# Kernel tuning notes

Hardware: AMD Instinct MI355X
Metric: run time of the kernel (lower is better)

The kernel has to match this reference:

```python
import jax, jax.numpy as jnp
import numpy as np

N_NODES = 4096

def _gcn_conv(x, edge_index, W, b):
    # PyG GCNConv: x' = D^-1/2 (A + I) D^-1/2 (x @ W) + b
    n = x.shape[0]
    self_loops = jnp.arange(n, dtype=edge_index.dtype)
    src = jnp.concatenate([edge_index[0], self_loops])  # message sources
    dst = jnp.concatenate([edge_index[1], self_loops])  # aggregation targets
    xw = x @ W  # [N, 8]
    deg = jax.ops.segment_sum(jnp.ones_like(dst, dtype=xw.dtype), dst, num_segments=n)
    dinv = jnp.where(deg > 0, jax.lax.rsqrt(deg), 0.0)
    norm = dinv[src] * dinv[dst]  # [E+N]
    msg = xw[src] * norm[:, None]  # gather + scale
    out = jax.ops.segment_sum(msg, dst, num_segments=n)  # scatter-add
    return out + b


def setup_inputs() -> dict:
    key = jax.random.key(0)
    k1, k2, k3, k4 = jax.random.split(key, 4)
    n, e, y_dim, hid = N_NODES, 131072, 4096, 8
    x = jax.random.normal(k1, (n, 1), dtype=jnp.float32)
    edge_index = jax.random.randint(k2, (2, e), 0, n, dtype=jnp.int64)
    W1 = jax.random.normal(k3, (1, hid), dtype=jnp.float32)  # fan_in=1
    b1 = jnp.zeros((hid,), dtype=jnp.float32)
    Wr = jax.random.normal(k4, (n * hid, y_dim), dtype=jnp.float32) / np.sqrt(n * hid)
    br = jnp.zeros((y_dim,), dtype=jnp.float32)
    return {"x": x, "edge_index": edge_index, "W1": W1, "b1": b1, "Wr": Wr, "br": br}


def reference(x, edge_index, W1, b1, Wr, br):
    h = _gcn_conv(x, edge_index, W1, b1)        # [N, 8]
    h = jax.nn.relu(h.reshape(-1))               # [N*8]
    return h @ Wr + br                           # [y_dim]
```

## Files before the change

### kernel.cpp

```cpp
#include <hip/hip_runtime.h>

#define N_NODES 4096
#define HID 8
#define N_EDGES 131072
#define YDIM 4096
#define K_TOT (N_NODES * HID)
#define KC 128
#define GEMV_BLOCK 256

__global__ __launch_bounds__(256) void k_init(float* __restrict__ deg,
                                              float* __restrict__ t,
                                              float* __restrict__ out,
                                              const float* __restrict__ br) {
  int i = blockIdx.x * blockDim.x + threadIdx.x;
  if (i < N_NODES) { deg[i] = 1.0f; t[i] = 0.0f; }
  if (i < YDIM) out[i] = br[i];
}

__global__ __launch_bounds__(256) void k_deg(const int* __restrict__ ei,
                                             float* __restrict__ deg) {
  int e = blockIdx.x * blockDim.x + threadIdx.x;
  if (e < N_EDGES) {
    int d = ei[N_EDGES + e];
    atomicAdd(&deg[d], 1.0f);
  }
}

__global__ __launch_bounds__(256) void k_dinv(const float* __restrict__ deg,
                                              float* __restrict__ dinv) {
  int i = blockIdx.x * blockDim.x + threadIdx.x;
  if (i < N_NODES) dinv[i] = rsqrtf(deg[i]);
}

__global__ __launch_bounds__(256) void k_scatter(const int* __restrict__ ei,
                                                 const float* __restrict__ x,
                                                 const float* __restrict__ dinv,
                                                 float* __restrict__ t) {
  int e = blockIdx.x * blockDim.x + threadIdx.x;
  if (e < N_EDGES) {
    int s = ei[e];
    int d = ei[N_EDGES + e];
    atomicAdd(&t[d], x[s] * dinv[s]);
  }
}

__global__ __launch_bounds__(256) void k_h(const float* __restrict__ x,
                                           const float* __restrict__ dinv,
                                           const float* __restrict__ t,
                                           const float* __restrict__ W1,
                                           const float* __restrict__ b1,
                                           float* __restrict__ h) {
  int i = blockIdx.x * blockDim.x + threadIdx.x;
  if (i < N_NODES) {
    float di = dinv[i];
    float s = di * (t[i] + x[i] * di);
#pragma unroll
    for (int j = 0; j < HID; ++j) {
      float v = s * W1[j] + b1[j];
      h[i * HID + j] = v > 0.0f ? v : 0.0f;
    }
  }
}

__global__ __launch_bounds__(GEMV_BLOCK) void k_gemv(const float* __restrict__ Wr,
                                                     const float* __restrict__ h,
                                                     float* __restrict__ out) {
  __shared__ float hs[KC];
  __shared__ int ks[KC];
  __shared__ int cnt;
  const int tid = threadIdx.x;
  const int cg = blockIdx.x & 3;
  const int ck = blockIdx.x >> 2;
  const int k0 = ck * KC;

  if (tid == 0) cnt = 0;
  __syncthreads();
  if (tid < KC) {
    float v = h[k0 + tid];
    if (v != 0.0f) {
      int p = atomicAdd(&cnt, 1);
      hs[p] = v;
      ks[p] = tid;
    }
  }
  __syncthreads();

  const int n = cnt;
  const int col = cg * (GEMV_BLOCK * 4) + tid * 4;
  const float* base = Wr + (size_t)k0 * YDIM + col;
  float ax = 0.f, ay = 0.f, az = 0.f, aw = 0.f;
  for (int q = 0; q < n; ++q) {
    float hv = hs[q];
    int kk = ks[q];
    const float4 w = *(const float4*)(base + (size_t)kk * YDIM);
    ax += hv * w.x;
    ay += hv * w.y;
    az += hv * w.z;
    aw += hv * w.w;
  }
  atomicAdd(&out[col + 0], ax);
  atomicAdd(&out[col + 1], ay);
  atomicAdd(&out[col + 2], az);
  atomicAdd(&out[col + 3], aw);
}

extern "C" void kernel_launch(void* const* d_in, const int* in_sizes, int n_in,
                              void* d_out, int out_size, void* d_ws, size_t ws_size,
                              hipStream_t stream) {
  const float* x  = (const float*)d_in[0];
  const int*   ei = (const int*)d_in[1];
  const float* W1 = (const float*)d_in[2];
  const float* b1 = (const float*)d_in[3];
  const float* Wr = (const float*)d_in[4];
  const float* br = (const float*)d_in[5];
  float* out = (float*)d_out;

  float* deg  = (float*)d_ws;
  float* dinv = deg + N_NODES;
  float* t    = dinv + N_NODES;
  float* h    = t + N_NODES;

  k_init   <<<(N_NODES + 255) / 256, 256, 0, stream>>>(deg, t, out, br);
  k_deg    <<<(N_EDGES + 255) / 256, 256, 0, stream>>>(ei, deg);
  k_dinv   <<<(N_NODES + 255) / 256, 256, 0, stream>>>(deg, dinv);
  k_scatter<<<(N_EDGES + 255) / 256, 256, 0, stream>>>(ei, x, dinv, t);
  k_h      <<<(N_NODES + 255) / 256, 256, 0, stream>>>(x, dinv, t, W1, b1, h);
  k_gemv   <<<4 * (K_TOT / KC), GEMV_BLOCK, 0, stream>>>(Wr, h, out);
}
```

Baseline: 677.4 us.

## Globally compact nonzero ReLU outputs and unroll sparse GEMV for more loads in flight

The hidden-activation kernel now builds one global list of positive ReLU entries, storing their row offsets and values through an atomic counter. The GEMV splits that list evenly across 256 chunks, replacing the old per-block shared-memory compaction of fixed 128-row slices. This balances work between blocks. The inner loop is unrolled by four with separate accumulators so more float4 loads of Wr are outstanding at once. The cost is an extra global atomic per node, row order that varies from run to run, and a fixed shared buffer of 160 entries that assumes no chunk gets more than that.

Measured after the change: 687.1 us. No clear change (+1.4%).

```diff
diff --git a/kernel.cpp b/kernel.cpp
--- a/kernel.cpp
+++ b/kernel.cpp
@@ -5,25 +5,23 @@
 #define N_EDGES 131072
 #define YDIM 4096
 #define K_TOT (N_NODES * HID)
-#define KC 128
+#define NCHUNK 256
 #define GEMV_BLOCK 256
 
 __global__ __launch_bounds__(256) void k_init(float* __restrict__ deg,
                                               float* __restrict__ t,
                                               float* __restrict__ out,
-                                              const float* __restrict__ br) {
+                                              const float* __restrict__ br,
+                                              int* __restrict__ nnz) {
   int i = blockIdx.x * blockDim.x + threadIdx.x;
-  if (i < N_NODES) { deg[i] = 1.0f; t[i] = 0.0f; }
-  if (i < YDIM) out[i] = br[i];
+  if (i < N_NODES) { deg[i] = 1.0f; t[i] = 0.0f; out[i] = br[i]; }
+  if (i == 0) *nnz = 0;
 }
 
 __global__ __launch_bounds__(256) void k_deg(const int* __restrict__ ei,
                                              float* __restrict__ deg) {
   int e = blockIdx.x * blockDim.x + threadIdx.x;
-  if (e < N_EDGES) {
-    int d = ei[N_EDGES + e];
-    atomicAdd(&deg[d], 1.0f);
-  }
+  if (e < N_EDGES) atomicAdd(&deg[ei[N_EDGES + e]], 1.0f);
 }
 
 __global__ __launch_bounds__(256) void k_dinv(const float* __restrict__ deg,
@@ -44,64 +42,82 @@
   }
 }
 
-__global__ __launch_bounds__(256) void k_h(const float* __restrict__ x,
-                                           const float* __restrict__ dinv,
-                                           const float* __restrict__ t,
-                                           const float* __restrict__ W1,
-                                           const float* __restrict__ b1,
-                                           float* __restrict__ h) {
+__global__ __launch_bounds__(256) void k_hc(const float* __restrict__ x,
+                                            const float* __restrict__ dinv,
+                                            const float* __restrict__ t,
+                                            const float* __restrict__ W1,
+                                            const float* __restrict__ b1,
+                                            int* __restrict__ nnz,
+                                            int* __restrict__ nzk,
+                                            float* __restrict__ nzv) {
   int i = blockIdx.x * blockDim.x + threadIdx.x;
-  if (i < N_NODES) {
-    float di = dinv[i];
-    float s = di * (t[i] + x[i] * di);
+  if (i >= N_NODES) return;
+  float di = dinv[i];
+  float s = di * (t[i] + x[i] * di);
+  float v[HID];
+  int nloc = 0;
 #pragma unroll
-    for (int j = 0; j < HID; ++j) {
-      float v = s * W1[j] + b1[j];
-      h[i * HID + j] = v > 0.0f ? v : 0.0f;
+  for (int j = 0; j < HID; ++j) {
+    float u = s * W1[j] + b1[j];
+    v[j] = u;
+    nloc += (u > 0.0f) ? 1 : 0;
+  }
+  int p = atomicAdd(nnz, nloc);
+#pragma unroll
+  for (int j = 0; j < HID; ++j) {
+    if (v[j] > 0.0f) {
+      nzk[p] = (i * HID + j) * YDIM;
+      nzv[p] = v[j];
+      ++p;
     }
   }
 }
 
 __global__ __launch_bounds__(GEMV_BLOCK) void k_gemv(const float* __restrict__ Wr,
-                                                     const float* __restrict__ h,
+                                                     const int* __restrict__ nnzp,
+                                                     const int* __restrict__ nzk,
+                                                     const float* __restrict__ nzv,
                                                      float* __restrict__ out) {
-  __shared__ float hs[KC];
-  __shared__ int ks[KC];
-  __shared__ int cnt;
+  __shared__ float hs[160];
+  __shared__ int ks[160];
   const int tid = threadIdx.x;
   const int cg = blockIdx.x & 3;
   const int ck = blockIdx.x >> 2;
-  const int k0 = ck * KC;
-
-  if (tid == 0) cnt = 0;
-  __syncthreads();
-  if (tid < KC) {
-    float v = h[k0 + tid];
-    if (v != 0.0f) {
-      int p = atomicAdd(&cnt, 1);
-      hs[p] = v;
-      ks[p] = tid;
-    }
-  }
+  const int nnz = *nnzp;
+  const int qs = (ck * nnz) >> 8;
+  const int qe = ((ck + 1) * nnz) >> 8;
+  const int cnt = qe - qs;
+  if (tid < cnt) { hs[tid] = nzv[qs + tid]; ks[tid] = nzk[qs + tid]; }
   __syncthreads();
 
-  const int n = cnt;
   const int col = cg * (GEMV_BLOCK * 4) + tid * 4;
-  const float* base = Wr + (size_t)k0 * YDIM + col;
-  float ax = 0.f, ay = 0.f, az = 0.f, aw = 0.f;
-  for (int q = 0; q < n; ++q) {
-    float hv = hs[q];
-    int kk = ks[q];
-    const float4 w = *(const float4*)(base + (size_t)kk * YDIM);
-    ax += hv * w.x;
-    ay += hv * w.y;
-    az += hv * w.z;
-    aw += hv * w.w;
+  const float* base = Wr + col;
+  float4 a0 = {0, 0, 0, 0}, a1 = {0, 0, 0, 0}, a2 = {0, 0, 0, 0}, a3 = {0, 0, 0, 0};
+  int q = 0;
+  for (; q + 4 <= cnt; q += 4) {
+    float h0 = hs[q], h1 = hs[q + 1], h2 = hs[q + 2], h3 = hs[q + 3];
+    const float4 w0 = *(const float4*)(base + (size_t)(unsigned)ks[q]);
+    const float4 w1 = *(const float4*)(base + (size_t)(unsigned)ks[q + 1]);
+    const float4 w2 = *(const float4*)(base + (size_t)(unsigned)ks[q + 2]);
+    const float4 w3 = *(const float4*)(base + (size_t)(unsigned)ks[q + 3]);
+    a0.x += h0 * w0.x; a0.y += h0 * w0.y; a0.z += h0 * w0.z; a0.w += h0 * w0.w;
+    a1.x += h1 * w1.x; a1.y += h1 * w1.y; a1.z += h1 * w1.z; a1.w += h1 * w1.w;
+    a2.x += h2 * w2.x; a2.y += h2 * w2.y; a2.z += h2 * w2.z; a2.w += h2 * w2.w;
+    a3.x += h3 * w3.x; a3.y += h3 * w3.y; a3.z += h3 * w3.z; a3.w += h3 * w3.w;
   }
-  atomicAdd(&out[col + 0], ax);
-  atomicAdd(&out[col + 1], ay);
-  atomicAdd(&out[col + 2], az);
-  atomicAdd(&out[col + 3], aw);
+  for (; q < cnt; ++q) {
+    float h0 = hs[q];
+    const float4 w0 = *(const float4*)(base + (size_t)(unsigned)ks[q]);
+    a0.x += h0 * w0.x; a0.y += h0 * w0.y; a0.z += h0 * w0.z; a0.w += h0 * w0.w;
+  }
+  float rx = a0.x + a1.x + a2.x + a3.x;
+  float ry = a0.y + a1.y + a2.y + a3.y;
+  float rz = a0.z + a1.z + a2.z + a3.z;
+  float rw = a0.w + a1.w + a2.w + a3.w;
+  atomicAdd(&out[col + 0], rx);
+  atomicAdd(&out[col + 1], ry);
+  atomicAdd(&out[col + 2], rz);
+  atomicAdd(&out[col + 3], rw);
 }
 
 extern "C" void kernel_launch(void* const* d_in, const int* in_sizes, int n_in,
@@ -118,12 +134,14 @@
   float* deg  = (float*)d_ws;
   float* dinv = deg + N_NODES;
   float* t    = dinv + N_NODES;
-  float* h    = t + N_NODES;
+  int*   nnz  = (int*)(t + N_NODES);
+  int*   nzk  = nnz + 16;
+  float* nzv  = (float*)(nzk + K_TOT);
 
-  k_init   <<<(N_NODES + 255) / 256, 256, 0, stream>>>(deg, t, out, br);
+  k_init   <<<(N_NODES + 255) / 256, 256, 0, stream>>>(deg, t, out, br, nnz);
   k_deg    <<<(N_EDGES + 255) / 256, 256, 0, stream>>>(ei, deg);
   k_dinv   <<<(N_NODES + 255) / 256, 256, 0, stream>>>(deg, dinv);
   k_scatter<<<(N_EDGES + 255) / 256, 256, 0, stream>>>(ei, x, dinv, t);
-  k_h      <<<(N_NODES + 255) / 256, 256, 0, stream>>>(x, dinv, t, W1, b1, h);
-  k_gemv   <<<4 * (K_TOT / KC), GEMV_BLOCK, 0, stream>>>(Wr, h, out);
+  k_hc     <<<(N_NODES + 255) / 256, 256, 0, stream>>>(x, dinv, t, W1, b1, nnz, nzk, nzv);
+  k_gemv   <<<4 * NCHUNK, GEMV_BLOCK, 0, stream>>>(Wr, nnz, nzk, nzv, out);
 }
```
